# Kernel optimization log

Hardware: AMD Instinct MI355X
Metric: run time of the kernel (lower is better)

The kernel has to match this reference:

```python
import jax, jax.numpy as jnp
import numpy as np

ATOM_DIM = 128; RBF_DIM = 32; GEOM_HID = 128; SCAT = 64; OUT = 64; CUTOFF = 5.0
MAX_Z = 100; Z_EMB = 32; E_DIM = 32; PAIR_HID = 64
B = 16; N = 64; P = 8000; NE = 80


def _lin(key, i, o):
    kw, kb = jax.random.split(key)
    W = jax.random.normal(kw, (i, o), jnp.float32) / np.sqrt(i).astype(np.float32)
    b = jax.random.normal(kb, (o,), jnp.float32) * 0.01
    return W, b


def setup_inputs() -> dict:
    key = jax.random.key(0)
    ks = jax.random.split(key, 24)
    inp = {}
    inp["h_flat"] = jax.random.normal(ks[0], (B * N, ATOM_DIM), jnp.float32)
    inp["z_flat"] = jax.random.randint(ks[1], (B * N,), 0, MAX_Z + 1)
    inp["e_feat"] = jax.random.normal(ks[2], (NE, E_DIM), jnp.float32)
    inp["path_j"] = jax.random.randint(ks[3], (P,), 0, B * N)
    inp["path_k"] = jax.random.randint(ks[4], (P,), 0, B * N)
    # distances in (0, 1.2*cutoff) so some paths exceed the cutoff
    inp["path_r0j"] = jax.random.uniform(ks[5], (P,), jnp.float32, 0.1, 1.2 * CUTOFF)
    inp["path_r0k"] = jax.random.uniform(ks[6], (P,), jnp.float32, 0.1, 1.2 * CUTOFF)
    inp["path_rjk"] = jax.random.uniform(ks[7], (P,), jnp.float32, 0.1, 1.2 * CUTOFF)
    inp["path_cosangle"] = jax.random.uniform(ks[8], (P,), jnp.float32, -1.0, 1.0)
    inp["path_batch"] = jnp.sort(jax.random.randint(ks[9], (P,), 0, B))
    inp["bsz"] = B
    # params
    inp["z_emb"] = jax.random.normal(ks[10], (MAX_Z + 1, Z_EMB), jnp.float32)
    pe_in = 2 * Z_EMB + E_DIM
    inp["pe_w1"], inp["pe_b1"] = _lin(ks[11], pe_in, PAIR_HID)
    inp["pe_w2"], inp["pe_b2"] = _lin(ks[12], PAIR_HID, PAIR_HID)
    inp["pe_w3"], inp["pe_b3"] = _lin(ks[13], PAIR_HID, SCAT)
    gm_in = 2 * ATOM_DIM + 3 * RBF_DIM + 1
    inp["gm_w1"], inp["gm_b1"] = _lin(ks[14], gm_in, GEOM_HID)
    inp["gm_w2"], inp["gm_b2"] = _lin(ks[15], GEOM_HID, GEOM_HID)
    inp["gm_w3"], inp["gm_b3"] = _lin(ks[16], GEOM_HID, SCAT)
    inp["op_w1"], inp["op_b1"] = _lin(ks[17], SCAT, GEOM_HID)
    inp["op_w2"], inp["op_b2"] = _lin(ks[18], GEOM_HID, OUT)
    return inp


def _rbf(r):
    centers = jnp.linspace(0.0, CUTOFF, RBF_DIM)
    width = centers[1] - centers[0]
    return jnp.exp(-0.5 * ((r[..., None] - centers) / width) ** 2)


def _cutoff_fn(r):
    return 0.5 * (jnp.cos(jnp.pi * r / CUTOFF) + 1.0) * (r < CUTOFF)


def _mlp3(x, w1, b1, w2, b2, w3, b3):
    h = jax.nn.silu(x @ w1 + b1)
    h = jax.nn.silu(h @ w2 + b2)
    return h @ w3 + b3


def _mlp2(x, w1, b1, w2, b2):
    return jax.nn.silu(x @ w1 + b1) @ w2 + b2


def reference(h_flat, z_flat, e_feat, path_j, path_k, path_r0j, path_r0k,
              path_rjk, path_cosangle, path_batch, bsz, z_emb,
              pe_w1, pe_b1, pe_w2, pe_b2, pe_w3, pe_b3,
              gm_w1, gm_b1, gm_w2, gm_b2, gm_w3, gm_b3,
              op_w1, op_b1, op_w2, op_b2):
    n_e = e_feat.shape[0]
    n_p = path_j.shape[0]
    # gather atom features
    hj = h_flat[path_j]                                  # (P, atom_dim)
    hk = h_flat[path_k]
    f0j = _rbf(jnp.minimum(path_r0j, CUTOFF))            # (P, rbf_dim)
    f0k = _rbf(jnp.minimum(path_r0k, CUTOFF))
    fjk = _rbf(jnp.minimum(path_rjk, CUTOFF))
    geom_in = jnp.concatenate([hj, hk, f0j, f0k, fjk, path_cosangle[:, None]], axis=-1)
    g_geom = _mlp3(geom_in, gm_w1, gm_b1, gm_w2, gm_b2, gm_w3, gm_b3)  # (P, scat)
    # element-pair energy features
    ej = z_emb[z_flat[path_j]]                           # (P, z_emb)
    ek = z_emb[z_flat[path_k]]
    pair_in = jnp.concatenate([
        jnp.broadcast_to(ej[:, None, :], (n_p, n_e, ej.shape[-1])),
        jnp.broadcast_to(ek[:, None, :], (n_p, n_e, ek.shape[-1])),
        jnp.broadcast_to(e_feat[None, :, :], (n_p, n_e, e_feat.shape[-1])),
    ], axis=-1)                                          # (P, nE, 2*z_emb+e_dim)
    g_elem = _mlp3(pair_in, pe_w1, pe_b1, pe_w2, pe_b2, pe_w3, pe_b3)  # (P, nE, scat)
    # cutoff weights and outer-product contribution
    cw = _cutoff_fn(path_r0j) * _cutoff_fn(path_r0k) * _cutoff_fn(path_rjk)  # (P,)
    contrib = g_geom[:, None, :] * g_elem * cw[:, None, None]          # (P, nE, scat)
    # scatter-add into batch bins
    agg = jax.ops.segment_sum(contrib, path_batch, num_segments=bsz)   # (B, nE, scat)
    norm = jax.ops.segment_sum(cw, path_batch, num_segments=bsz)       # (B,)
    agg = agg / jnp.maximum(norm, 1e-8)[:, None, None]
    return _mlp2(agg, op_w1, op_b1, op_w2, op_b2)                      # (B, nE, out)
```

## Files before the change

### kernel.cpp

```cpp
#include <hip/hip_runtime.h>
#include <math.h>

typedef float f32x4 __attribute__((ext_vector_type(4)));
typedef short bf16x8 __attribute__((ext_vector_type(8)));
typedef unsigned short u16;

#define RBF_DIM 32
#define CUTOFF 5.0f
#define PI_F 3.14159265358979323846f
#define BB 16
#define PP 8000
#define NEE 80

#define CW_OFF      0
#define GCW_OFF     8000
#define AGG_OFF     520000
#define ZEJW_OFF    601920
#define ZEKW_OFF    608384
#define EFWB_OFF    614848
#define NORM_OFF    619968
#define AIDX_OFF    619984
#define ZJA_OFF     627984
#define ZKA_OFF     635984
#define BOFF_OFF    643984
#define BCNT_OFF    644004
#define BSUM_OFF    644036
#define BCNTB_OFF   644548
#define BLKOFF_OFF  645060
#define CHS_OFF     645096
#define CHC_OFF     645362
#define CHB_OFF     645628
#define NC_OFF      645894
#define W2THI_OFF   645896
#define W2TLO_OFF   647944
#define W3THI_OFF   649992
#define W3TLO_OFF   652040
#define PJA_OFF     654088
#define PKA_OFF     662088
#define CWA_OFF     670088
#define HHI_OFF     678088
#define HLO_OFF     743624
#define GW1JKH_OFF  809160
#define GW1JKL_OFF  825544
#define GW1RH_OFF   841928
#define GW1RL_OFF   850120
#define GW2H_OFF    858312
#define GW2L_OFF    866504
#define GW3H_OFF    874696
#define GW3L_OFF    878792
#define HJW_OFF     882888
#define HKW_OFF     1013960

__device__ __forceinline__ float siluf(float x) { return x / (1.f + __expf(-x)); }
__device__ __forceinline__ float cutoff_fn(float r) {
    return (r < CUTOFF) ? 0.5f * (cosf(PI_F * r / CUTOFF) + 1.f) : 0.f;
}
__device__ __forceinline__ float rbff(float r, int i) {
    r = fminf(r, CUTOFF);
    float a = r * (31.0f / CUTOFF) - (float)i;
    return __expf(-0.5f * a * a);
}
__device__ __forceinline__ u16 f2bf_rne(float x) {
    unsigned u = __float_as_uint(x);
    return (u16)((u + 0x7FFFu + ((u >> 16) & 1u)) >> 16);
}
__device__ __forceinline__ unsigned cvtpk2(float a, float b) {
    unsigned r;
    asm("v_cvt_pk_bf16_f32 %0, %1, %2" : "=v"(r) : "v"(a), "v"(b));
    return r;
}
__device__ __forceinline__ void splitpack8(const float* xs, bf16x8& hi, bf16x8& lo) {
    union { bf16x8 v; unsigned u[4]; } H, L;
    #pragma unroll
    for (int d = 0; d < 4; ++d) {
        float a = xs[2 * d], b = xs[2 * d + 1];
        unsigned h = cvtpk2(a, b);
        float ra = a - __uint_as_float(h << 16);
        float rb = b - __uint_as_float(h & 0xFFFF0000u);
        H.u[d] = h;
        L.u[d] = cvtpk2(ra, rb);
    }
    hi = H.v; lo = L.v;
}

__global__ __launch_bounds__(256) void k0a_k1(
    const float* r0j, const float* r0k, const float* rjk, const int* pbatch,
    const float* z_emb, const float* e_feat, const float* pe_w1, const float* pe_b1,
    const float* pe_w2, const float* pe_w3,
    const float* h_flat, const float* gm_w1, const float* gm_w2, const float* gm_w3,
    float* ws, int* wsi)
{
    __shared__ float cwL[256];
    __shared__ int bL[256];
    __shared__ int redC[256];
    __shared__ float embL[4 * 32];
    int blkAll = blockIdx.x, t = threadIdx.x;
    if (blkAll < 32) {
        int bi = blkAll;
        for (int i = t; i < 2560; i += 256) ws[AGG_OFF + bi*2560 + i] = 0.f;
        int p = bi*250 + t;
        float cw = 0.f; int bin = -1; int valid = 0;
        if (t < 250) {
            cw = cutoff_fn(r0j[p]) * cutoff_fn(r0k[p]) * cutoff_fn(rjk[p]);
            ws[CW_OFF + p] = cw;
            bin = pbatch[p];
            valid = (cw > 0.f) ? 1 : 0;
        }
        cwL[t] = cw; bL[t] = bin; redC[t] = valid;
        __syncthreads();
        if (t < 16) {
            float s = 0.f; int c2 = 0;
            for (int i = 0; i < 256; ++i) {
                bool m = (bL[i] == t);
                s += m ? cwL[i] : 0.f;
                c2 += (m && cwL[i] > 0.f) ? 1 : 0;
            }
            ws[BSUM_OFF + bi*16 + t] = s;
            wsi[BCNTB_OFF + bi*16 + t] = c2;
        }
        __syncthreads();
        for (int s = 128; s > 0; s >>= 1) {
            if (t < s) redC[t] += redC[t + s];
            __syncthreads();
        }
        if (t == 0) wsi[BCNT_OFF + bi] = redC[0];
        return;
    }
    if (blkAll >= 106) {
        int blk = blkAll - 106;
        if (blk < 32) {
            u16* hh = (u16*)(ws + HHI_OFF);
            u16* hl = (u16*)(ws + HLO_OFF);
            int base = blk * 4096;
            for (int idx = t; idx < 4096; idx += 256) {
                int e = base + idx;
                float v = h_flat[e];
                u16 h = f2bf_rne(v);
                hh[e] = h;
                hl[e] = f2bf_rne(v - __uint_as_float(((unsigned)h) << 16));
            }
        } else if (blk < 34) {
            u16* wh = (u16*)(ws + GW1JKH_OFF);
            u16* wl = (u16*)(ws + GW1JKL_OFF);
            int base = (blk - 32) * 16384;
            for (int idx = t; idx < 16384; idx += 256) {
                int e = base + idx;
                int m = e >> 7, k = e & 127;
                float v = gm_w1[((m < 128) ? k : (128 + k)) * 128 + (m & 127)];
                u16 h = f2bf_rne(v);
                wh[e] = h;
                wl[e] = f2bf_rne(v - __uint_as_float(((unsigned)h) << 16));
            }
        } else if (blk == 34) {
            u16* wh = (u16*)(ws + GW1RH_OFF);
            u16* wl = (u16*)(ws + GW1RL_OFF);
            for (int e = t; e < 16384; e += 256) {
                int m = e >> 7, k = e & 127;
                float v = (k < 97) ? gm_w1[(256 + k) * 128 + m] : 0.f;
                u16 h = f2bf_rne(v);
                wh[e] = h;
                wl[e] = f2bf_rne(v - __uint_as_float(((unsigned)h) << 16));
            }
        } else if (blk == 35) {
            u16* wh = (u16*)(ws + GW2H_OFF);
            u16* wl = (u16*)(ws + GW2L_OFF);
            for (int e = t; e < 16384; e += 256) {
                int m = e >> 7, k = e & 127;
                float v = gm_w2[k * 128 + m];
                u16 h = f2bf_rne(v);
                wh[e] = h;
                wl[e] = f2bf_rne(v - __uint_as_float(((unsigned)h) << 16));
            }
        } else {
            u16* wh = (u16*)(ws + GW3H_OFF);
            u16* wl = (u16*)(ws + GW3L_OFF);
            for (int e = t; e < 8192; e += 256) {
                int m = e >> 7, k = e & 127;
                float v = gm_w3[k * 64 + m];
                u16 h = f2bf_rne(v);
                wh[e] = h;
                wl[e] = f2bf_rne(v - __uint_as_float(((unsigned)h) << 16));
            }
        }
        return;
    }
    int blk = blkAll - 32;
    if (blk >= 72) {
        const float* W = (blk == 72) ? pe_w2 : pe_w3;
        u16* hiD = (u16*)(ws + ((blk == 72) ? W2THI_OFF : W3THI_OFF));
        u16* loD = (u16*)(ws + ((blk == 72) ? W2TLO_OFF : W3TLO_OFF));
        for (int idx = t; idx < 4096; idx += 256) {
            int k = idx >> 6, n = idx & 63;
            float v = W[idx];
            u16 h = f2bf_rne(v);
            float hf = __uint_as_float(((unsigned)h) << 16);
            hiD[n*64 + k] = h;
            loD[n*64 + k] = f2bf_rne(v - hf);
        }
        return;
    }
    int r0, nrows, wbase;
    const float* src;
    float* dst;
    bool addb = false;
    if (blk < 26)      { r0 = blk * 4;        nrows = 101; src = z_emb;  wbase = 0;  dst = ws + ZEJW_OFF; }
    else if (blk < 52) { r0 = (blk - 26) * 4; nrows = 101; src = z_emb;  wbase = 32; dst = ws + ZEKW_OFF; }
    else               { r0 = (blk - 52) * 4; nrows = NEE; src = e_feat; wbase = 64; dst = ws + EFWB_OFF; addb = true; }
    if (t < 128) {
        int rl = t >> 5, i = t & 31;
        int r = r0 + rl;
        embL[t] = (r < nrows) ? src[r * 32 + i] : 0.f;
    }
    __syncthreads();
    int rl = t >> 6, c = t & 63;
    float acc = addb ? pe_b1[c] : 0.f;
    #pragma unroll
    for (int i = 0; i < 32; ++i)
        acc = fmaf(embL[rl * 32 + i], pe_w1[(wbase + i) * 64 + c], acc);
    int r = r0 + rl;
    if (r < nrows) dst[r * 64 + c] = acc;
}

__global__ __launch_bounds__(256) void k0b(float* ws, int* wsi)
{
    __shared__ int bcntL[32];
    __shared__ int cntB[16];
    __shared__ int boff[17];
    __shared__ int chkoff[17];
    int t = threadIdx.x;
    if (t < 16) {
        float s = 0.f;
        #pragma unroll 4
        for (int bi = 0; bi < 32; ++bi) s += ws[BSUM_OFF + bi*16 + t];
        ws[NORM_OFF + t] = s;
    }
    if (t >= 32 && t < 48) {
        int b = t - 32;
        int cb = 0;
        #pragma unroll 4
        for (int bi = 0; bi < 32; ++bi) cb += wsi[BCNTB_OFF + bi*16 + b];
        cntB[b] = cb;
    }
    if (t >= 64 && t < 96) bcntL[t - 64] = wsi[BCNT_OFF + (t - 64)];
    __syncthreads();
    for (int off = 1; off < 32; off <<= 1) {
        int v = (t < 32 && t >= off) ? bcntL[t - off] : 0;
        __syncthreads();
        if (t < 32) bcntL[t] += v;
        __syncthreads();
    }
    if (t < 32) wsi[BLKOFF_OFF + t] = bcntL[t] - wsi[BCNT_OFF + t];
    if (t == 0) {
        wsi[BLKOFF_OFF + 32] = bcntL[31];
        int bo = 0, co = 0;
        for (int b = 0; b < 16; ++b) {
            boff[b] = bo; chkoff[b] = co;
            bo += cntB[b];
            co += (cntB[b] + 31) >> 5;
        }
        boff[16] = bo; chkoff[16] = co;
        wsi[NC_OFF] = co;
    }
    __syncthreads();
    int NCv = chkoff[16];
    for (int ci = t; ci < NCv; ci += 256) {
        int b = 0;
        while (chkoff[b + 1] <= ci) b++;
        int local = ci - chkoff[b];
        int rem = cntB[b] - local * 32;
        wsi[CHS_OFF + ci] = boff[b] + local * 32;
        wsi[CHC_OFF + ci] = (rem < 32) ? rem : 32;
        wsi[CHB_OFF + ci] = b;
    }
}

__global__ __launch_bounds__(256) void k0c_k1b(
    const int* pj, const int* pk, const int* zf, float* ws, int* wsi)
{
    __shared__ int sc[256];
    int blk = blockIdx.x, t = threadIdx.x;
    if (blk < 32) {
        int bi = blk;
        int p = bi*250 + t;
        int valid = (t < 250 && ws[CW_OFF + p] > 0.f) ? 1 : 0;
        sc[t] = valid;
        __syncthreads();
        for (int off = 1; off < 256; off <<= 1) {
            int v = (t >= off) ? sc[t - off] : 0;
            __syncthreads();
            sc[t] += v;
            __syncthreads();
        }
        if (valid) {
            int pos = wsi[BLKOFF_OFF + bi] + sc[t] - 1;
            int pjv = pj[p], pkv = pk[p];
            wsi[AIDX_OFF + pos] = p;
            wsi[ZJA_OFF + pos] = zf[pjv];
            wsi[ZKA_OFF + pos] = zf[pkv];
            wsi[PJA_OFF + pos] = pjv;
            wsi[PKA_OFF + pos] = pkv;
            ws[CWA_OFF + pos] = ws[CW_OFF + p];
        }
        return;
    }
    int a0 = (blk - 32) * 64;
    int lane = t & 63, w = t >> 6, c = lane & 15, g = lane >> 4;
    const u16* hh = (const u16*)(ws + HHI_OFF);
    const u16* hl = (const u16*)(ws + HLO_OFF);
    const u16* wh = (const u16*)(ws + GW1JKH_OFF);
    const u16* wl = (const u16*)(ws + GW1JKL_OFF);
    f32x4 acc[4][4];
    #pragma unroll
    for (int i = 0; i < 4; ++i)
        #pragma unroll
        for (int j = 0; j < 4; ++j) acc[i][j] = (f32x4){0.f, 0.f, 0.f, 0.f};
    #pragma unroll 1
    for (int ks = 0; ks < 4; ++ks) {
        bf16x8 Ah[4], Al[4], Bh[4], Bl[4];
        #pragma unroll
        for (int mt = 0; mt < 4; ++mt) {
            int off = (w * 64 + mt * 16 + c) * 128 + ks * 32 + g * 8;
            Ah[mt] = *(const bf16x8*)(wh + off);
            Al[mt] = *(const bf16x8*)(wl + off);
        }
        #pragma unroll
        for (int nt = 0; nt < 4; ++nt) {
            int off = (a0 + nt * 16 + c) * 128 + ks * 32 + g * 8;
            Bh[nt] = *(const bf16x8*)(hh + off);
            Bl[nt] = *(const bf16x8*)(hl + off);
        }
        #pragma unroll
        for (int mt = 0; mt < 4; ++mt)
            #pragma unroll
            for (int nt = 0; nt < 4; ++nt) {
                f32x4 d = acc[mt][nt];
                d = __builtin_amdgcn_mfma_f32_16x16x32_bf16(Ah[mt], Bh[nt], d, 0, 0, 0);
                d = __builtin_amdgcn_mfma_f32_16x16x32_bf16(Ah[mt], Bl[nt], d, 0, 0, 0);
                d = __builtin_amdgcn_mfma_f32_16x16x32_bf16(Al[mt], Bh[nt], d, 0, 0, 0);
                acc[mt][nt] = d;
            }
    }
    float* dst = ws + ((w < 2) ? HJW_OFF : HKW_OFF);
    #pragma unroll
    for (int mt = 0; mt < 4; ++mt)
        #pragma unroll
        for (int nt = 0; nt < 4; ++nt) {
            int m = (w & 1) * 64 + mt * 16 + g * 4;
            int a = a0 + nt * 16 + c;
            *(f32x4*)(dst + a * 128 + m) = acc[mt][nt];
        }
}

__global__ __launch_bounds__(256) void k2_geom_mfma(
    const float* r0jG, const float* r0kG, const float* rjkG, const float* cosG,
    const float* b1g, const float* b2g, const float* b3g,
    float* ws, const int* wsi, float* gcw)
{
    __shared__ __align__(16) float sum3L[32 * 128];
    __shared__ __align__(16) u16 rbfH[4096], rbfL[4096];
    __shared__ __align__(16) u16 h1H[4096], h1L[4096];
    __shared__ __align__(16) u16 h2H[4096], h2L[4096];
    __shared__ int pjS[32], pkS[32];
    __shared__ float cwS[32], r0jS[32], r0kS[32], rjkS[32], cosS[32];

    int NC = wsi[NC_OFF];
    int cid = blockIdx.x;
    if (cid >= NC) return;
    int cs = wsi[CHS_OFF + cid], cnt = wsi[CHC_OFF + cid];
    int t = threadIdx.x, lane = t & 63, w = t >> 6, c = lane & 15, g = lane >> 4;

    if (t < 32) {
        int ap = cs + min(t, cnt - 1);
        int a = wsi[AIDX_OFF + ap];
        pjS[t] = wsi[PJA_OFF + ap]; pkS[t] = wsi[PKA_OFF + ap];
        cwS[t] = ws[CWA_OFF + ap];
        r0jS[t] = r0jG[a]; r0kS[t] = r0kG[a]; rjkS[t] = rjkG[a]; cosS[t] = cosG[a];
    }
    __syncthreads();
    {
        int p = t >> 3, kc = (t & 7) * 16;
        const float* rj = ws + HJW_OFF + pjS[p] * 128 + kc;
        const float* rk = ws + HKW_OFF + pkS[p] * 128 + kc;
        #pragma unroll
        for (int q = 0; q < 4; ++q) {
            f32x4 v = *(const f32x4*)(rj + q * 4) + *(const f32x4*)(rk + q * 4);
            *(f32x4*)(sum3L + ((p * 128 + kc + q * 4) ^ ((p & 7) << 2))) = v;
        }
    }
    {
        int p = t >> 3, k0 = (t & 7) * 16;
        float r0jv = r0jS[p], r0kv = r0kS[p], rjkv = rjkS[p], cv = cosS[p];
        #pragma unroll
        for (int hf = 0; hf < 2; ++hf) {
            int kb = k0 + hf * 8;
            float xs[8];
            #pragma unroll
            for (int i = 0; i < 8; ++i) {
                int k = kb + i;
                float v;
                if (k < 32) v = rbff(r0jv, k);
                else if (k < 64) v = rbff(r0kv, k - 32);
                else if (k < 96) v = rbff(rjkv, k - 64);
                else if (k == 96) v = cv;
                else v = 0.f;
                xs[i] = v;
            }
            bf16x8 hi, lo;
            splitpack8(xs, hi, lo);
            int idx = (p * 128 + kb) ^ ((p & 7) << 3);
            *(bf16x8*)(rbfH + idx) = hi;
            *(bf16x8*)(rbfL + idx) = lo;
        }
    }
    __syncthreads();

    const u16* w1h = (const u16*)(ws + GW1RH_OFF);
    const u16* w1l = (const u16*)(ws + GW1RL_OFF);
    const u16* w2h = (const u16*)(ws + GW2H_OFF);
    const u16* w2l = (const u16*)(ws + GW2L_OFF);
    const u16* w3h = (const u16*)(ws + GW3H_OFF);
    const u16* w3l = (const u16*)(ws + GW3L_OFF);

    f32x4 acc[2][2];
    #pragma unroll
    for (int i = 0; i < 2; ++i)
        #pragma unroll
        for (int j = 0; j < 2; ++j) acc[i][j] = (f32x4){0.f, 0.f, 0.f, 0.f};
    #pragma unroll 1
    for (int ks = 0; ks < 4; ++ks) {
        bf16x8 Ah[2], Al[2], Bh[2], Bl[2];
        #pragma unroll
        for (int ml = 0; ml < 2; ++ml) {
            int off = ((w * 2 + ml) * 16 + c) * 128 + ks * 32 + g * 8;
            Ah[ml] = *(const bf16x8*)(w1h + off);
            Al[ml] = *(const bf16x8*)(w1l + off);
        }
        #pragma unroll
        for (int nt = 0; nt < 2; ++nt) {
            int p = nt * 16 + c;
            int idx = (p * 128 + ks * 32 + g * 8) ^ ((p & 7) << 3);
            Bh[nt] = *(const bf16x8*)(rbfH + idx);
            Bl[nt] = *(const bf16x8*)(rbfL + idx);
        }
        #pragma unroll
        for (int ml = 0; ml < 2; ++ml)
            #pragma unroll
            for (int nt = 0; nt < 2; ++nt) {
                f32x4 d = acc[ml][nt];
                d = __builtin_amdgcn_mfma_f32_16x16x32_bf16(Ah[ml], Bh[nt], d, 0, 0, 0);
                d = __builtin_amdgcn_mfma_f32_16x16x32_bf16(Ah[ml], Bl[nt], d, 0, 0, 0);
                d = __builtin_amdgcn_mfma_f32_16x16x32_bf16(Al[ml], Bh[nt], d, 0, 0, 0);
// ... 44 lines not shown
            Bh[nt] = *(const bf16x8*)(h1H + idx);
            Bl[nt] = *(const bf16x8*)(h1L + idx);
        }
        #pragma unroll
        for (int ml = 0; ml < 2; ++ml)
            #pragma unroll
            for (int nt = 0; nt < 2; ++nt) {
                f32x4 d = acc[ml][nt];
                d = __builtin_amdgcn_mfma_f32_16x16x32_bf16(Ah[ml], Bh[nt], d, 0, 0, 0);
                d = __builtin_amdgcn_mfma_f32_16x16x32_bf16(Ah[ml], Bl[nt], d, 0, 0, 0);
                d = __builtin_amdgcn_mfma_f32_16x16x32_bf16(Al[ml], Bh[nt], d, 0, 0, 0);
                acc[ml][nt] = d;
            }
    }
    #pragma unroll
    for (int ml = 0; ml < 2; ++ml)
        #pragma unroll
        for (int nt = 0; nt < 2; ++nt) {
            int p = nt * 16 + c;
            int m0 = (w * 2 + ml) * 16 + g * 4;
            f32x4 bb = *(const f32x4*)(b2g + m0);
            f32x4 x = acc[ml][nt] + bb;
            float v0 = siluf(x[0]), v1 = siluf(x[1]), v2 = siluf(x[2]), v3 = siluf(x[3]);
            unsigned h01 = cvtpk2(v0, v1), h23 = cvtpk2(v2, v3);
            float l0 = v0 - __uint_as_float(h01 << 16);
            float l1 = v1 - __uint_as_float(h01 & 0xFFFF0000u);
            float l2 = v2 - __uint_as_float(h23 << 16);
            float l3 = v3 - __uint_as_float(h23 & 0xFFFF0000u);
            unsigned lo01 = cvtpk2(l0, l1), lo23 = cvtpk2(l2, l3);
            int idx = (p * 128 + m0) ^ ((p & 7) << 3);
            uint2 uh; uh.x = h01; uh.y = h23;
            uint2 ul; ul.x = lo01; ul.y = lo23;
            *(uint2*)(h2H + idx) = uh;
            *(uint2*)(h2L + idx) = ul;
        }
    __syncthreads();

    f32x4 acc3[2];
    acc3[0] = (f32x4){0.f, 0.f, 0.f, 0.f};
    acc3[1] = (f32x4){0.f, 0.f, 0.f, 0.f};
    #pragma unroll 1
    for (int ks = 0; ks < 4; ++ks) {
        bf16x8 Ah, Al, Bh[2], Bl[2];
        {
            int off = (w * 16 + c) * 128 + ks * 32 + g * 8;
            Ah = *(const bf16x8*)(w3h + off);
            Al = *(const bf16x8*)(w3l + off);
        }
        #pragma unroll
        for (int nt = 0; nt < 2; ++nt) {
            int p = nt * 16 + c;
            int idx = (p * 128 + ks * 32 + g * 8) ^ ((p & 7) << 3);
            Bh[nt] = *(const bf16x8*)(h2H + idx);
            Bl[nt] = *(const bf16x8*)(h2L + idx);
        }
        #pragma unroll
        for (int nt = 0; nt < 2; ++nt) {
            f32x4 d = acc3[nt];
            d = __builtin_amdgcn_mfma_f32_16x16x32_bf16(Ah, Bh[nt], d, 0, 0, 0);
            d = __builtin_amdgcn_mfma_f32_16x16x32_bf16(Ah, Bl[nt], d, 0, 0, 0);
            d = __builtin_amdgcn_mfma_f32_16x16x32_bf16(Al, Bh[nt], d, 0, 0, 0);
            acc3[nt] = d;
        }
    }
    {
        int m0 = w * 16 + g * 4;
        f32x4 bb = *(const f32x4*)(b3g + m0);
        #pragma unroll
        for (int nt = 0; nt < 2; ++nt) {
            int p = nt * 16 + c;
            if (p < cnt) {
                f32x4 o = (acc3[nt] + bb) * cwS[p];
                *(f32x4*)(gcw + (cs + p) * 64 + m0) = o;
            }
        }
    }
}

__global__ __launch_bounds__(256) void k3_pair_mfma(
    const float* ws, const int* wsi, const float* gcw, float* agg,
    const float* b2g, const float* b3g)
{
    __shared__ __align__(16) float sL[32 * 64];
    __shared__ __align__(16) u16 h2buf[4][2048];
    __shared__ __align__(16) u16 a2lL[4096];
    __shared__ __align__(16) u16 a3lL[4096];

    int NC = wsi[NC_OFF];
    int bid = blockIdx.x;
    int cid = bid / 10;
    int et  = bid - cid * 10;
    if (cid >= NC) return;
    int cs  = wsi[CHS_OFF + cid];
    int cnt = wsi[CHC_OFF + cid];
    int bb  = wsi[CHB_OFF + cid];

    int t = threadIdx.x;
    int lane = t & 63, w = t >> 6;
    int c = lane & 15, g = lane >> 4;

    {
        int p = t >> 3, kc = (t & 7) * 8;
        int ap = cs + min(p, cnt - 1);
        int zj = wsi[ZJA_OFF + ap], zk = wsi[ZKA_OFF + ap];
        const f32x4* rj = (const f32x4*)(ws + ZEJW_OFF + zj * 64 + kc);
        const f32x4* rk = (const f32x4*)(ws + ZEKW_OFF + zk * 64 + kc);
        int sw = (p & 7) << 2;
        *(f32x4*)(sL + ((p * 64 + kc) ^ sw))     = rj[0] + rk[0];
        *(f32x4*)(sL + ((p * 64 + kc + 4) ^ sw)) = rj[1] + rk[1];
    }
    {
        const unsigned* s2 = (const unsigned*)(ws + W2TLO_OFF);
        const unsigned* s3 = (const unsigned*)(ws + W3TLO_OFF);
        unsigned* d2 = (unsigned*)a2lL;
        unsigned* d3 = (unsigned*)a3lL;
        #pragma unroll
        for (int rr = 0; rr < 8; ++rr) {
            int i = rr * 256 + t;
            int sw = ((i >> 5) & 7) << 2;
            d2[i ^ sw] = s2[i];
            d3[i ^ sw] = s3[i];
        }
    }
    const u16* w2hi = (const u16*)(ws + W2THI_OFF);
    const u16* w3hi = (const u16*)(ws + W3THI_OFF);
    bf16x8 A2h[4][2], A3h[4][2];
    #pragma unroll
    for (int mt = 0; mt < 4; ++mt)
        #pragma unroll
        for (int ks = 0; ks < 2; ++ks) {
            int off = (mt * 16 + c) * 64 + ks * 32 + g * 8;
            A2h[mt][ks] = *(const bf16x8*)(w2hi + off);
            A3h[mt][ks] = *(const bf16x8*)(w3hi + off);
        }
    __syncthreads();

    u16* myh = h2buf[w];
    u16* myl = h2buf[w] + 1024;
    const float* efp = ws + EFWB_OFF;
    const int aswz = (c & 7) << 3;

    const int cb64 = c * 64;
    const int wk0 = (g * 8) ^ aswz;
    const int wk1 = (32 + g * 8) ^ aswz;
    const int s48 = aswz & 48, s8 = aswz & 8;
    const int hwb = cb64 + ((4 * g) ^ s8);
    const u16* a2p = a2lL + cb64;
    const u16* a3p = a3lL + cb64;

    #pragma unroll 1
    for (int ei = 0; ei < 2; ++ei) {
        int e = et * 8 + w * 2 + ei;
        float part[16];
        #pragma unroll
        for (int i = 0; i < 16; ++i) part[i] = 0.f;

        #pragma unroll 1
        for (int nt = 0; nt < 2; ++nt) {
            int p = nt * 16 + c;
            int psw = (p & 7) << 2;
            f32x4 gvr[4];
            {
                int pc = cs + min(p, cnt - 1);
                #pragma unroll
                for (int mt = 0; mt < 4; ++mt)
                    gvr[mt] = *(const f32x4*)(gcw + pc * 64 + mt * 16 + 4 * g);
            }
            f32x4 acc4[4];
            #pragma unroll
            for (int mt = 0; mt < 4; ++mt) acc4[mt] = (f32x4){0.f, 0.f, 0.f, 0.f};
            #pragma unroll
            for (int ks = 0; ks < 2; ++ks) {
                f32x4 e0 = *(const f32x4*)(efp + e * 64 + ks * 32 + g * 8);
                f32x4 e1 = *(const f32x4*)(efp + e * 64 + ks * 32 + g * 8 + 4);
                int base = p * 64 + ks * 32 + g * 8;
                f32x4 x0 = *(const f32x4*)(sL + (base ^ psw));
                f32x4 x1 = *(const f32x4*)(sL + ((base + 4) ^ psw));
                x0 += e0; x1 += e1;
                float xs[8];
                #pragma unroll
                for (int i = 0; i < 4; ++i) { xs[i] = siluf(x0[i]); xs[4 + i] = siluf(x1[i]); }
                bf16x8 Bh, Bl;
                splitpack8(xs, Bh, Bl);
                const int wk = ks ? wk1 : wk0;
                #pragma unroll
                for (int mt = 0; mt < 4; ++mt) {
                    bf16x8 a2l = *(const bf16x8*)(a2p + wk + mt * 1024);
                    f32x4 d = acc4[mt];
                    d = __builtin_amdgcn_mfma_f32_16x16x32_bf16(A2h[mt][ks], Bh, d, 0, 0, 0);
                    d = __builtin_amdgcn_mfma_f32_16x16x32_bf16(A2h[mt][ks], Bl, d, 0, 0, 0);
                    d = __builtin_amdgcn_mfma_f32_16x16x32_bf16(a2l,         Bh, d, 0, 0, 0);
                    acc4[mt] = d;
                }
            }
            #pragma unroll
            for (int mt = 0; mt < 4; ++mt) {
                f32x4 b2v = *(const f32x4*)(b2g + mt * 16 + 4 * g);
                f32x4 h = acc4[mt] + b2v;
                float v0 = siluf(h[0]), v1 = siluf(h[1]), v2 = siluf(h[2]), v3 = siluf(h[3]);
                unsigned h01 = cvtpk2(v0, v1), h23 = cvtpk2(v2, v3);
                float l0 = v0 - __uint_as_float(h01 << 16);
                float l1 = v1 - __uint_as_float(h01 & 0xFFFF0000u);
                float l2 = v2 - __uint_as_float(h23 << 16);
                float l3 = v3 - __uint_as_float(h23 & 0xFFFF0000u);
                unsigned lo01 = cvtpk2(l0, l1), lo23 = cvtpk2(l2, l3);
                int idx = hwb + ((mt * 16) ^ s48);
                uint2 uh, ul;
                uh.x = h01; uh.y = h23;
                ul.x = lo01; ul.y = lo23;
                *(uint2*)(myh + idx) = uh;
                *(uint2*)(myl + idx) = ul;
                acc4[mt] = (f32x4){0.f, 0.f, 0.f, 0.f};
            }
            #pragma unroll
            for (int ks = 0; ks < 2; ++ks) {
                const int wk = ks ? wk1 : wk0;
                bf16x8 Ch = *(const bf16x8*)(myh + cb64 + wk);
                bf16x8 Cl = *(const bf16x8*)(myl + cb64 + wk);
                #pragma unroll
                for (int mt = 0; mt < 4; ++mt) {
                    bf16x8 a3l = *(const bf16x8*)(a3p + wk + mt * 1024);
                    f32x4 d = acc4[mt];
                    d = __builtin_amdgcn_mfma_f32_16x16x32_bf16(A3h[mt][ks], Ch, d, 0, 0, 0);
                    d = __builtin_amdgcn_mfma_f32_16x16x32_bf16(A3h[mt][ks], Cl, d, 0, 0, 0);
                    d = __builtin_amdgcn_mfma_f32_16x16x32_bf16(a3l,         Ch, d, 0, 0, 0);
                    acc4[mt] = d;
                }
            }
            float vmask = (p < cnt) ? 1.f : 0.f;
            #pragma unroll
            for (int mt = 0; mt < 4; ++mt) {
                f32x4 b3v = *(const f32x4*)(b3g + mt * 16 + 4 * g);
                f32x4 o = acc4[mt] + b3v;
                #pragma unroll
                for (int r = 0; r < 4; ++r) part[mt * 4 + r] += o[r] * gvr[mt][r] * vmask;
            }
        }
        #pragma unroll
        for (int i = 0; i < 16; ++i) {
            float v = part[i];
            v += __shfl_xor(v, 1, 64);
            v += __shfl_xor(v, 2, 64);
            v += __shfl_xor(v, 4, 64);
            v += __shfl_xor(v, 8, 64);
            part[i] = v;
        }
        int f = (c >> 2) * 16 + g * 4 + (c & 3);
        atomicAdd(agg + (bb * NEE + e) * 64 + f, part[c]);
    }
}

__global__ __launch_bounds__(256) void k4_out(
    const float* ws, const float* W1, const float* b1,
    const float* W2, const float* b2, float* out)
{
    __shared__ float xT[64][68];
    __shared__ float W1L[64 * 128];
    __shared__ float hTT[128][68];
    __shared__ float W2L[128 * 64];
    __shared__ float normL[16];
    int t = threadIdx.x;
    int gbase = blockIdx.x * 64;
    if (t < 16) normL[t] = 1.f / fmaxf(ws[NORM_OFF + t], 1e-8f);
    for (int idx = t; idx < 8192; idx += 256) { W1L[idx] = W1[idx]; W2L[idx] = W2[idx]; }
    __syncthreads();
    {
        int r = t & 63, cq = t >> 6;
        int gg = gbase + r;
        int b = gg / NEE;
        float rn = normL[b];
        const float* arow = ws + AGG_OFF + gg * 64 + cq * 16;
        #pragma unroll
        for (int q = 0; q < 4; ++q) {
            float4 v = *(const float4*)(arow + q * 4);
            int c = cq * 16 + q * 4;
            xT[c + 0][r] = v.x * rn; xT[c + 1][r] = v.y * rn;
            xT[c + 2][r] = v.z * rn; xT[c + 3][r] = v.w * rn;
        }
    }
    __syncthreads();
    {
        int tcx = t & 15, trx = t >> 4;
        int c0 = tcx * 8, r0 = trx * 4;
        float acc[4][8];
        #pragma unroll
        for (int j = 0; j < 4; ++j)
            #pragma unroll
            for (int q = 0; q < 8; ++q) acc[j][q] = 0.f;
        #pragma unroll 4
        for (int kk = 0; kk < 64; ++kk) {
            float4 x4 = *(const float4*)&xT[kk][r0];
            float4 wa = *(const float4*)&W1L[kk * 128 + c0];
            float4 wb = *(const float4*)&W1L[kk * 128 + c0 + 4];
            float x[4] = {x4.x, x4.y, x4.z, x4.w};
            float w[8] = {wa.x, wa.y, wa.z, wa.w, wb.x, wb.y, wb.z, wb.w};
            #pragma unroll
            for (int j = 0; j < 4; ++j)
                #pragma unroll
                for (int q = 0; q < 8; ++q)
                    acc[j][q] = fmaf(x[j], w[q], acc[j][q]);
        }
        #pragma unroll
        for (int q = 0; q < 8; ++q) {
            float bb = b1[c0 + q];
            float4 v;
            v.x = siluf(acc[0][q] + bb);
            v.y = siluf(acc[1][q] + bb);
            v.z = siluf(acc[2][q] + bb);
            v.w = siluf(acc[3][q] + bb);
            *(float4*)&hTT[c0 + q][r0] = v;
        }
    }
    __syncthreads();
    {
        int tcx = t & 7, trx = t >> 3;
        int c0 = tcx * 8, r0 = trx * 2;
        float acc[2][8];
        #pragma unroll
        for (int j = 0; j < 2; ++j)
            #pragma unroll
            for (int q = 0; q < 8; ++q) acc[j][q] = 0.f;
        #pragma unroll 4
        for (int kk = 0; kk < 128; ++kk) {
            float2 x2 = *(const float2*)&hTT[kk][r0];
            float4 wa = *(const float4*)&W2L[kk * 64 + c0];
            float4 wb = *(const float4*)&W2L[kk * 64 + c0 + 4];
            float w[8] = {wa.x, wa.y, wa.z, wa.w, wb.x, wb.y, wb.z, wb.w};
            #pragma unroll
            for (int q = 0; q < 8; ++q) {
                acc[0][q] = fmaf(x2.x, w[q], acc[0][q]);
                acc[1][q] = fmaf(x2.y, w[q], acc[1][q]);
            }
        }
        int gg = gbase + r0;
        #pragma unroll
        for (int j = 0; j < 2; ++j) {
            float o[8];
            #pragma unroll
            for (int q = 0; q < 8; ++q) o[q] = acc[j][q] + b2[c0 + q];
            *(float4*)&out[(gg + j) * 64 + c0] = make_float4(o[0], o[1], o[2], o[3]);
            *(float4*)&out[(gg + j) * 64 + c0 + 4] = make_float4(o[4], o[5], o[6], o[7]);
        }
    }
}

extern "C" void kernel_launch(void* const* d_in, const int* in_sizes, int n_in,
                              void* d_out, int out_size, void* d_ws, size_t ws_size,
                              hipStream_t stream) {
    (void)in_sizes; (void)n_in; (void)out_size; (void)ws_size;
    const float* h_flat = (const float*)d_in[0];
    const int*   z_flat = (const int*)d_in[1];
    const float* e_feat = (const float*)d_in[2];
    const int*   path_j = (const int*)d_in[3];
    const int*   path_k = (const int*)d_in[4];
    const float* r0j    = (const float*)d_in[5];
    const float* r0k    = (const float*)d_in[6];
    const float* rjk    = (const float*)d_in[7];
    const float* cosang = (const float*)d_in[8];
    const int*   pbatch = (const int*)d_in[9];
    const float* z_emb  = (const float*)d_in[11];
    const float* pe_w1  = (const float*)d_in[12];
    const float* pe_b1  = (const float*)d_in[13];
    const float* pe_w2  = (const float*)d_in[14];
    const float* pe_b2  = (const float*)d_in[15];
    const float* pe_w3  = (const float*)d_in[16];
    const float* pe_b3  = (const float*)d_in[17];
    const float* gm_w1  = (const float*)d_in[18];
    const float* gm_b1  = (const float*)d_in[19];
    const float* gm_w2  = (const float*)d_in[20];
    const float* gm_b2  = (const float*)d_in[21];
    const float* gm_w3  = (const float*)d_in[22];
    const float* gm_b3  = (const float*)d_in[23];
    const float* op_w1  = (const float*)d_in[24];
    const float* op_b1  = (const float*)d_in[25];
    const float* op_w2  = (const float*)d_in[26];
    const float* op_b2  = (const float*)d_in[27];

    float* ws  = (float*)d_ws;
    int*   wsi = (int*)d_ws;
    float* gcw = ws + GCW_OFF;
    float* agg = ws + AGG_OFF;

    hipLaunchKernelGGL(k0a_k1, dim3(143), dim3(256), 0, stream,
                       r0j, r0k, rjk, pbatch,
                       z_emb, e_feat, pe_w1, pe_b1, pe_w2, pe_w3,
                       h_flat, gm_w1, gm_w2, gm_w3, ws, wsi);
    hipLaunchKernelGGL(k0b, dim3(1), dim3(256), 0, stream, ws, wsi);
    hipLaunchKernelGGL(k0c_k1b, dim3(48), dim3(256), 0, stream,
                       path_j, path_k, z_flat, ws, wsi);
    hipLaunchKernelGGL(k2_geom_mfma, dim3(266), dim3(256), 0, stream,
                       r0j, r0k, rjk, cosang,
                       gm_b1, gm_b2, gm_b3, ws, wsi, gcw);
    hipLaunchKernelGGL(k3_pair_mfma, dim3(2660), dim3(256), 0, stream,
                       ws, wsi, gcw, agg, pe_b2, pe_b3);
    hipLaunchKernelGGL(k4_out, dim3(20), dim3(256), 0, stream,
                       ws, op_w1, op_b1, op_w2, op_b2, (float*)d_out);
}
```

Before: 134.8 us.

## Split pair-MLP work to one energy per wave and use a transpose-style reduction

```diff
diff --git a/kernel.cpp b/kernel.cpp
--- a/kernel.cpp
+++ b/kernel.cpp
@@ -583,8 +583,8 @@
 
     int NC = wsi[NC_OFF];
     int bid = blockIdx.x;
-    int cid = bid / 10;
-    int et  = bid - cid * 10;
+    int cid = bid / 20;
+    int et  = bid - cid * 20;
     if (cid >= NC) return;
     int cs  = wsi[CHS_OFF + cid];
     int cnt = wsi[CHC_OFF + cid];
@@ -628,6 +628,12 @@
             A2h[mt][ks] = *(const bf16x8*)(w2hi + off);
             A3h[mt][ks] = *(const bf16x8*)(w3hi + off);
         }
+    f32x4 b2f[4], b3f[4];
+    #pragma unroll
+    for (int mt = 0; mt < 4; ++mt) {
+        b2f[mt] = *(const f32x4*)(b2g + mt * 16 + 4 * g);
+        b3f[mt] = *(const f32x4*)(b3g + mt * 16 + 4 * g);
+    }
     __syncthreads();
 
     u16* myh = h2buf[w];
@@ -643,106 +649,121 @@
     const u16* a2p = a2lL + cb64;
     const u16* a3p = a3lL + cb64;
 
+    int e = et * 4 + w;
+    float part[16];
+    #pragma unroll
+    for (int i = 0; i < 16; ++i) part[i] = 0.f;
+
+    f32x4 ef00 = *(const f32x4*)(efp + e * 64 + g * 8);
+    f32x4 ef01 = *(const f32x4*)(efp + e * 64 + g * 8 + 4);
+    f32x4 ef10 = *(const f32x4*)(efp + e * 64 + 32 + g * 8);
+    f32x4 ef11 = *(const f32x4*)(efp + e * 64 + 32 + g * 8 + 4);
+
     #pragma unroll 1
-    for (int ei = 0; ei < 2; ++ei) {
-        int e = et * 8 + w * 2 + ei;
-        float part[16];
-        #pragma unroll
-        for (int i = 0; i < 16; ++i) part[i] = 0.f;
-
-        #pragma unroll 1
-        for (int nt = 0; nt < 2; ++nt) {
-            int p = nt * 16 + c;
-            int psw = (p & 7) << 2;
-            f32x4 gvr[4];
-            {
-                int pc = cs + min(p, cnt - 1);
-                #pragma unroll
-                for (int mt = 0; mt < 4; ++mt)
-                    gvr[mt] = *(const f32x4*)(gcw + pc * 64 + mt * 16 + 4 * g);
-            }
-            f32x4 acc4[4];
-            #pragma unroll
-            for (int mt = 0; mt < 4; ++mt) acc4[mt] = (f32x4){0.f, 0.f, 0.f, 0.f};
-            #pragma unroll
-            for (int ks = 0; ks < 2; ++ks) {
-                f32x4 e0 = *(const f32x4*)(efp + e * 64 + ks * 32 + g * 8);
-                f32x4 e1 = *(const f32x4*)(efp + e * 64 + ks * 32 + g * 8 + 4);
-                int base = p * 64 + ks * 32 + g * 8;
-                f32x4 x0 = *(const f32x4*)(sL + (base ^ psw));
-                f32x4 x1 = *(const f32x4*)(sL + ((base + 4) ^ psw));
-                x0 += e0; x1 += e1;
-                float xs[8];
-                #pragma unroll
-                for (int i = 0; i < 4; ++i) { xs[i] = siluf(x0[i]); xs[4 + i] = siluf(x1[i]); }
-                bf16x8 Bh, Bl;
-                splitpack8(xs, Bh, Bl);
-                const int wk = ks ? wk1 : wk0;
-                #pragma unroll
-                for (int mt = 0; mt < 4; ++mt) {
-                    bf16x8 a2l = *(const bf16x8*)(a2p + wk + mt * 1024);
-                    f32x4 d = acc4[mt];
-                    d = __builtin_amdgcn_mfma_f32_16x16x32_bf16(A2h[mt][ks], Bh, d, 0, 0, 0);
-                    d = __builtin_amdgcn_mfma_f32_16x16x32_bf16(A2h[mt][ks], Bl, d, 0, 0, 0);
-                    d = __builtin_amdgcn_mfma_f32_16x16x32_bf16(a2l,         Bh, d, 0, 0, 0);
-                    acc4[mt] = d;
-                }
-            }
+    for (int nt = 0; nt < 2; ++nt) {
+        int p = nt * 16 + c;
+        int psw = (p & 7) << 2;
+        f32x4 gvr[4];
+        {
+            int pc = cs + min(p, cnt - 1);
+            #pragma unroll
+            for (int mt = 0; mt < 4; ++mt)
+                gvr[mt] = *(const f32x4*)(gcw + pc * 64 + mt * 16 + 4 * g);
+        }
+        f32x4 acc4[4];
+        #pragma unroll
+        for (int mt = 0; mt < 4; ++mt) acc4[mt] = (f32x4){0.f, 0.f, 0.f, 0.f};
+        #pragma unroll
+        for (int ks = 0; ks < 2; ++ks) {
+            const int wk = ks ? wk1 : wk0;
+            f32x4 e0 = ks ? ef10 : ef00;
+            f32x4 e1 = ks ? ef11 : ef01;
+            int base = p * 64 + ks * 32 + g * 8;
+            f32x4 x0 = *(const f32x4*)(sL + (base ^ psw));
+            f32x4 x1 = *(const f32x4*)(sL + ((base + 4) ^ psw));
+            x0 += e0; x1 += e1;
+            float xs[8];
+            #pragma unroll
+            for (int i = 0; i < 4; ++i) { xs[i] = siluf(x0[i]); xs[4 + i] = siluf(x1[i]); }
+            bf16x8 Bh, Bl;
+            splitpack8(xs, Bh, Bl);
             #pragma unroll
             for (int mt = 0; mt < 4; ++mt) {
-                f32x4 b2v = *(const f32x4*)(b2g + mt * 16 + 4 * g);
-                f32x4 h = acc4[mt] + b2v;
-                float v0 = siluf(h[0]), v1 = siluf(h[1]), v2 = siluf(h[2]), v3 = siluf(h[3]);
-                unsigned h01 = cvtpk2(v0, v1), h23 = cvtpk2(v2, v3);
-                float l0 = v0 - __uint_as_float(h01 << 16);
-                float l1 = v1 - __uint_as_float(h01 & 0xFFFF0000u);
-                float l2 = v2 - __uint_as_float(h23 << 16);
-                float l3 = v3 - __uint_as_float(h23 & 0xFFFF0000u);
-                unsigned lo01 = cvtpk2(l0, l1), lo23 = cvtpk2(l2, l3);
-                int idx = hwb + ((mt * 16) ^ s48);
-                uint2 uh, ul;
-                uh.x = h01; uh.y = h23;
-                ul.x = lo01; ul.y = lo23;
-                *(uint2*)(myh + idx) = uh;
-                *(uint2*)(myl + idx) = ul;
-                acc4[mt] = (f32x4){0.f, 0.f, 0.f, 0.f};
-            }
-            #pragma unroll
-            for (int ks = 0; ks < 2; ++ks) {
-                const int wk = ks ? wk1 : wk0;
-                bf16x8 Ch = *(const bf16x8*)(myh + cb64 + wk);
-                bf16x8 Cl = *(const bf16x8*)(myl + cb64 + wk);
-                #pragma unroll
-                for (int mt = 0; mt < 4; ++mt) {
-                    bf16x8 a3l = *(const bf16x8*)(a3p + wk + mt * 1024);
-                    f32x4 d = acc4[mt];
-                    d = __builtin_amdgcn_mfma_f32_16x16x32_bf16(A3h[mt][ks], Ch, d, 0, 0, 0);
-                    d = __builtin_amdgcn_mfma_f32_16x16x32_bf16(A3h[mt][ks], Cl, d, 0, 0, 0);
-                    d = __builtin_amdgcn_mfma_f32_16x16x32_bf16(a3l,         Ch, d, 0, 0, 0);
-                    acc4[mt] = d;
-                }
-            }
-            float vmask = (p < cnt) ? 1.f : 0.f;
+                bf16x8 a2l = *(const bf16x8*)(a2p + wk + mt * 1024);
+                f32x4 d = acc4[mt];
+                d = __builtin_amdgcn_mfma_f32_16x16x32_bf16(A2h[mt][ks], Bh, d, 0, 0, 0);
+                d = __builtin_amdgcn_mfma_f32_16x16x32_bf16(A2h[mt][ks], Bl, d, 0, 0, 0);
+                d = __builtin_amdgcn_mfma_f32_16x16x32_bf16(a2l,         Bh, d, 0, 0, 0);
+                acc4[mt] = d;
+            }
+        }
+        #pragma unroll
+        for (int mt = 0; mt < 4; ++mt) {
+            f32x4 h = acc4[mt] + b2f[mt];
+            float v0 = siluf(h[0]), v1 = siluf(h[1]), v2 = siluf(h[2]), v3 = siluf(h[3]);
+            unsigned h01 = cvtpk2(v0, v1), h23 = cvtpk2(v2, v3);
+            float l0 = v0 - __uint_as_float(h01 << 16);
+            float l1 = v1 - __uint_as_float(h01 & 0xFFFF0000u);
+            float l2 = v2 - __uint_as_float(h23 << 16);
+            float l3 = v3 - __uint_as_float(h23 & 0xFFFF0000u);
+            unsigned lo01 = cvtpk2(l0, l1), lo23 = cvtpk2(l2, l3);
+            int idx = hwb + ((mt * 16) ^ s48);
+            uint2 uh, ul;
+            uh.x = h01; uh.y = h23;
+            ul.x = lo01; ul.y = lo23;
+            *(uint2*)(myh + idx) = uh;
+            *(uint2*)(myl + idx) = ul;
+            acc4[mt] = (f32x4){0.f, 0.f, 0.f, 0.f};
+        }
+        #pragma unroll
+        for (int ks = 0; ks < 2; ++ks) {
+            const int wk = ks ? wk1 : wk0;
+            bf16x8 Ch = *(const bf16x8*)(myh + cb64 + wk);
+            bf16x8 Cl = *(const bf16x8*)(myl + cb64 + wk);
             #pragma unroll
             for (int mt = 0; mt < 4; ++mt) {
-                f32x4 b3v = *(const f32x4*)(b3g + mt * 16 + 4 * g);
-                f32x4 o = acc4[mt] + b3v;
-                #pragma unroll
-                for (int r = 0; r < 4; ++r) part[mt * 4 + r] += o[r] * gvr[mt][r] * vmask;
-            }
-        }
-        #pragma unroll
-        for (int i = 0; i < 16; ++i) {
-            float v = part[i];
-            v += __shfl_xor(v, 1, 64);
-            v += __shfl_xor(v, 2, 64);
-            v += __shfl_xor(v, 4, 64);
-            v += __shfl_xor(v, 8, 64);
-            part[i] = v;
-        }
-        int f = (c >> 2) * 16 + g * 4 + (c & 3);
-        atomicAdd(agg + (bb * NEE + e) * 64 + f, part[c]);
-    }
+                bf16x8 a3l = *(const bf16x8*)(a3p + wk + mt * 1024);
+                f32x4 d = acc4[mt];
+                d = __builtin_amdgcn_mfma_f32_16x16x32_bf16(A3h[mt][ks], Ch, d, 0, 0, 0);
+                d = __builtin_amdgcn_mfma_f32_16x16x32_bf16(A3h[mt][ks], Cl, d, 0, 0, 0);
+                d = __builtin_amdgcn_mfma_f32_16x16x32_bf16(a3l,         Ch, d, 0, 0, 0);
+                acc4[mt] = d;
+            }
+        }
+        float vmask = (p < cnt) ? 1.f : 0.f;
+        #pragma unroll
+        for (int mt = 0; mt < 4; ++mt) {
+            f32x4 o = acc4[mt] + b3f[mt];
+            #pragma unroll
+            for (int r = 0; r < 4; ++r) part[mt * 4 + r] += o[r] * gvr[mt][r] * vmask;
+        }
+    }
+    float v8[8];
+    #pragma unroll
+    for (int j = 0; j < 8; ++j) {
+        float keep = (c & 8) ? part[j + 8] : part[j];
+        float send = (c & 8) ? part[j] : part[j + 8];
+        v8[j] = keep + __shfl_xor(send, 8, 64);
+    }
+    float v4[4];
+    #pragma unroll
+    for (int j = 0; j < 4; ++j) {
+        float keep = (c & 4) ? v8[j + 4] : v8[j];
+        float send = (c & 4) ? v8[j] : v8[j + 4];
+        v4[j] = keep + __shfl_xor(send, 4, 64);
+    }
+    float v2[2];
+    #pragma unroll
+    for (int j = 0; j < 2; ++j) {
+        float keep = (c & 2) ? v4[j + 2] : v4[j];
+        float send = (c & 2) ? v4[j] : v4[j + 2];
+        v2[j] = keep + __shfl_xor(send, 2, 64);
+    }
+    float keep1 = (c & 1) ? v2[1] : v2[0];
+    float send1 = (c & 1) ? v2[0] : v2[1];
+    float v1 = keep1 + __shfl_xor(send1, 1, 64);
+    int f = (c >> 2) * 16 + g * 4 + (c & 3);
+    atomicAdd(agg + (bb * NEE + e) * 64 + f, v1);
 }
 
 __global__ __launch_bounds__(256) void k4_out(
@@ -886,7 +907,7 @@
     hipLaunchKernelGGL(k2_geom_mfma, dim3(266), dim3(256), 0, stream,
                        r0j, r0k, rjk, cosang,
                        gm_b1, gm_b2, gm_b3, ws, wsi, gcw);
-    hipLaunchKernelGGL(k3_pair_mfma, dim3(2660), dim3(256), 0, stream,
+    hipLaunchKernelGGL(k3_pair_mfma, dim3(5320), dim3(256), 0, stream,
                        ws, wsi, gcw, agg, pe_b2, pe_b3);
     hipLaunchKernelGGL(k4_out, dim3(20), dim3(256), 0, stream,
                        ws, op_w1, op_b1, op_w2, op_b2, (float*)d_out);
```

Result: slower. 142.8 us (+5.9%).

## Replace scan-based compaction with atomic per-batch reservoirs and shuffle-based hidden exchange

Applied to the files above, without the earlier changes.

```diff
diff --git a/kernel.cpp b/kernel.cpp
--- a/kernel.cpp
+++ b/kernel.cpp
@@ -11,6 +11,7 @@
 #define BB 16
 #define PP 8000
 #define NEE 80
+#define RSZ 500
 
 #define CW_OFF      0
 #define GCW_OFF     8000
@@ -24,13 +25,6 @@
 #define ZKA_OFF     635984
 #define BOFF_OFF    643984
 #define BCNT_OFF    644004
-#define BSUM_OFF    644036
-#define BCNTB_OFF   644548
-#define BLKOFF_OFF  645060
-#define CHS_OFF     645096
-#define CHC_OFF     645362
-#define CHB_OFF     645628
-#define NC_OFF      645894
 #define W2THI_OFF   645896
 #define W2TLO_OFF   647944
 #define W3THI_OFF   649992
@@ -88,42 +82,42 @@
     const float* z_emb, const float* e_feat, const float* pe_w1, const float* pe_b1,
     const float* pe_w2, const float* pe_w3,
     const float* h_flat, const float* gm_w1, const float* gm_w2, const float* gm_w3,
+    const int* pj, const int* pk, const int* zf,
     float* ws, int* wsi)
 {
     __shared__ float cwL[256];
     __shared__ int bL[256];
-    __shared__ int redC[256];
     __shared__ float embL[4 * 32];
     int blkAll = blockIdx.x, t = threadIdx.x;
     if (blkAll < 32) {
         int bi = blkAll;
         for (int i = t; i < 2560; i += 256) ws[AGG_OFF + bi*2560 + i] = 0.f;
         int p = bi*250 + t;
-        float cw = 0.f; int bin = -1; int valid = 0;
+        float cw = 0.f; int bin = -1;
         if (t < 250) {
             cw = cutoff_fn(r0j[p]) * cutoff_fn(r0k[p]) * cutoff_fn(rjk[p]);
-            ws[CW_OFF + p] = cw;
             bin = pbatch[p];
-            valid = (cw > 0.f) ? 1 : 0;
-        }
-        cwL[t] = cw; bL[t] = bin; redC[t] = valid;
+            if (cw > 0.f) {
+                int pos = atomicAdd(&wsi[BCNT_OFF + bin], 1);
+                if (pos < RSZ) {
+                    int slot = bin * RSZ + pos;
+                    int pjv = pj[p], pkv = pk[p];
+                    wsi[AIDX_OFF + slot] = p;
+                    wsi[ZJA_OFF + slot] = zf[pjv];
+                    wsi[ZKA_OFF + slot] = zf[pkv];
+                    wsi[PJA_OFF + slot] = pjv;
+                    wsi[PKA_OFF + slot] = pkv;
+                    ws[CWA_OFF + slot] = cw;
+                }
+            }
+        }
+        cwL[t] = cw; bL[t] = bin;
         __syncthreads();
         if (t < 16) {
-            float s = 0.f; int c2 = 0;
-            for (int i = 0; i < 256; ++i) {
-                bool m = (bL[i] == t);
-                s += m ? cwL[i] : 0.f;
-                c2 += (m && cwL[i] > 0.f) ? 1 : 0;
-            }
-            ws[BSUM_OFF + bi*16 + t] = s;
-            wsi[BCNTB_OFF + bi*16 + t] = c2;
-        }
-        __syncthreads();
-        for (int s = 128; s > 0; s >>= 1) {
-            if (t < s) redC[t] += redC[t + s];
-            __syncthreads();
-        }
-        if (t == 0) wsi[BCNT_OFF + bi] = redC[0];
+            float s = 0.f;
+            for (int i = 0; i < 256; ++i) s += (bL[i] == t) ? cwL[i] : 0.f;
+            atomicAdd(ws + NORM_OFF + t, s);
+        }
         return;
     }
     if (blkAll >= 106) {
@@ -221,89 +215,10 @@
     if (r < nrows) dst[r * 64 + c] = acc;
 }
 
-__global__ __launch_bounds__(256) void k0b(float* ws, int* wsi)
+__global__ __launch_bounds__(256) void k1b_hw(float* ws)
 {
-    __shared__ int bcntL[32];
-    __shared__ int cntB[16];
-    __shared__ int boff[17];
-    __shared__ int chkoff[17];
     int t = threadIdx.x;
-    if (t < 16) {
-        float s = 0.f;
-        #pragma unroll 4
-        for (int bi = 0; bi < 32; ++bi) s += ws[BSUM_OFF + bi*16 + t];
-        ws[NORM_OFF + t] = s;
-    }
-    if (t >= 32 && t < 48) {
-        int b = t - 32;
-        int cb = 0;
-        #pragma unroll 4
-        for (int bi = 0; bi < 32; ++bi) cb += wsi[BCNTB_OFF + bi*16 + b];
-        cntB[b] = cb;
-    }
-    if (t >= 64 && t < 96) bcntL[t - 64] = wsi[BCNT_OFF + (t - 64)];
-    __syncthreads();
-    for (int off = 1; off < 32; off <<= 1) {
-        int v = (t < 32 && t >= off) ? bcntL[t - off] : 0;
-        __syncthreads();
-        if (t < 32) bcntL[t] += v;
-        __syncthreads();
-    }
-    if (t < 32) wsi[BLKOFF_OFF + t] = bcntL[t] - wsi[BCNT_OFF + t];
-    if (t == 0) {
-        wsi[BLKOFF_OFF + 32] = bcntL[31];
-        int bo = 0, co = 0;
-        for (int b = 0; b < 16; ++b) {
-            boff[b] = bo; chkoff[b] = co;
-            bo += cntB[b];
-            co += (cntB[b] + 31) >> 5;
-        }
-        boff[16] = bo; chkoff[16] = co;
-        wsi[NC_OFF] = co;
-    }
-    __syncthreads();
-    int NCv = chkoff[16];
-    for (int ci = t; ci < NCv; ci += 256) {
-        int b = 0;
-        while (chkoff[b + 1] <= ci) b++;
-        int local = ci - chkoff[b];
-        int rem = cntB[b] - local * 32;
-        wsi[CHS_OFF + ci] = boff[b] + local * 32;
-        wsi[CHC_OFF + ci] = (rem < 32) ? rem : 32;
-        wsi[CHB_OFF + ci] = b;
-    }
-}
-
-__global__ __launch_bounds__(256) void k0c_k1b(
-    const int* pj, const int* pk, const int* zf, float* ws, int* wsi)
-{
-    __shared__ int sc[256];
-    int blk = blockIdx.x, t = threadIdx.x;
-    if (blk < 32) {
-        int bi = blk;
-        int p = bi*250 + t;
-        int valid = (t < 250 && ws[CW_OFF + p] > 0.f) ? 1 : 0;
-        sc[t] = valid;
-        __syncthreads();
-        for (int off = 1; off < 256; off <<= 1) {
-            int v = (t >= off) ? sc[t - off] : 0;
-            __syncthreads();
-            sc[t] += v;
-            __syncthreads();
-        }
-        if (valid) {
-            int pos = wsi[BLKOFF_OFF + bi] + sc[t] - 1;
-            int pjv = pj[p], pkv = pk[p];
-            wsi[AIDX_OFF + pos] = p;
-            wsi[ZJA_OFF + pos] = zf[pjv];
-            wsi[ZKA_OFF + pos] = zf[pkv];
-            wsi[PJA_OFF + pos] = pjv;
-            wsi[PKA_OFF + pos] = pkv;
-            ws[CWA_OFF + pos] = ws[CW_OFF + p];
-        }
-        return;
-    }
-    int a0 = (blk - 32) * 64;
+    int a0 = blockIdx.x * 64;
     int lane = t & 63, w = t >> 6, c = lane & 15, g = lane >> 4;
     const u16* hh = (const u16*)(ws + HHI_OFF);
     const u16* hl = (const u16*)(ws + HLO_OFF);
@@ -363,10 +278,14 @@
     __shared__ int pjS[32], pkS[32];
     __shared__ float cwS[32], r0jS[32], r0kS[32], rjkS[32], cosS[32];
 
-    int NC = wsi[NC_OFF];
-    int cid = blockIdx.x;
-    if (cid >= NC) return;
-    int cs = wsi[CHS_OFF + cid], cnt = wsi[CHC_OFF + cid];
+    int bid = blockIdx.x;
+    int b = bid >> 4, ci = bid & 15;
+    int cntb = wsi[BCNT_OFF + b];
+    if (cntb > RSZ) cntb = RSZ;
+    int cs = b * RSZ + ci * 32;
+    int cnt = cntb - ci * 32;
+    if (cnt <= 0) return;
+    if (cnt > 32) cnt = 32;
     int t = threadIdx.x, lane = t & 63, w = t >> 6, c = lane & 15, g = lane >> 4;
 
     if (t < 32) {
@@ -577,18 +496,19 @@
     const float* b2g, const float* b3g)
 {
     __shared__ __align__(16) float sL[32 * 64];
-    __shared__ __align__(16) u16 h2buf[4][2048];
     __shared__ __align__(16) u16 a2lL[4096];
     __shared__ __align__(16) u16 a3lL[4096];
 
-    int NC = wsi[NC_OFF];
     int bid = blockIdx.x;
     int cid = bid / 10;
     int et  = bid - cid * 10;
-    if (cid >= NC) return;
-    int cs  = wsi[CHS_OFF + cid];
-    int cnt = wsi[CHC_OFF + cid];
-    int bb  = wsi[CHB_OFF + cid];
+    int bb = cid >> 4, ci = cid & 15;
+    int cntb = wsi[BCNT_OFF + bb];
+    if (cntb > RSZ) cntb = RSZ;
+    int cs = bb * RSZ + ci * 32;
+    int cnt = cntb - ci * 32;
+    if (cnt <= 0) return;
+    if (cnt > 32) cnt = 32;
 
     int t = threadIdx.x;
     int lane = t & 63, w = t >> 6;
@@ -630,16 +550,11 @@
         }
     __syncthreads();
 
-    u16* myh = h2buf[w];
-    u16* myl = h2buf[w] + 1024;
     const float* efp = ws + EFWB_OFF;
     const int aswz = (c & 7) << 3;
-
     const int cb64 = c * 64;
     const int wk0 = (g * 8) ^ aswz;
     const int wk1 = (32 + g * 8) ^ aswz;
-    const int s48 = aswz & 48, s8 = aswz & 8;
-    const int hwb = cb64 + ((4 * g) ^ s8);
     const u16* a2p = a2lL + cb64;
     const u16* a3p = a3lL + cb64;
 
@@ -688,37 +603,38 @@
                     acc4[mt] = d;
                 }
             }
+            float sv[4][4];
             #pragma unroll
             for (int mt = 0; mt < 4; ++mt) {
                 f32x4 b2v = *(const f32x4*)(b2g + mt * 16 + 4 * g);
                 f32x4 h = acc4[mt] + b2v;
-                float v0 = siluf(h[0]), v1 = siluf(h[1]), v2 = siluf(h[2]), v3 = siluf(h[3]);
-                unsigned h01 = cvtpk2(v0, v1), h23 = cvtpk2(v2, v3);
-                float l0 = v0 - __uint_as_float(h01 << 16);
-                float l1 = v1 - __uint_as_float(h01 & 0xFFFF0000u);
-                float l2 = v2 - __uint_as_float(h23 << 16);
-                float l3 = v3 - __uint_as_float(h23 & 0xFFFF0000u);
-                unsigned lo01 = cvtpk2(l0, l1), lo23 = cvtpk2(l2, l3);
-                int idx = hwb + ((mt * 16) ^ s48);
-                uint2 uh, ul;
-                uh.x = h01; uh.y = h23;
-                ul.x = lo01; ul.y = lo23;
-                *(uint2*)(myh + idx) = uh;
-                *(uint2*)(myl + idx) = ul;
+                #pragma unroll
+                for (int r = 0; r < 4; ++r) sv[mt][r] = siluf(h[r]);
                 acc4[mt] = (f32x4){0.f, 0.f, 0.f, 0.f};
+            }
+            bf16x8 Ch[2], Cl[2];
+            #pragma unroll
+            for (int ks = 0; ks < 2; ++ks) {
+                float v[8];
+                #pragma unroll
+                for (int i = 0; i < 8; ++i) {
+                    int sl = c + ((((g & 1) << 1) + (i >> 2)) << 4);
+                    float t0 = __shfl(sv[2 * ks][i & 3], sl, 64);
+                    float t1 = __shfl(sv[2 * ks + 1][i & 3], sl, 64);
+                    v[i] = (g >= 2) ? t1 : t0;
+                }
+                splitpack8(v, Ch[ks], Cl[ks]);
             }
             #pragma unroll
             for (int ks = 0; ks < 2; ++ks) {
                 const int wk = ks ? wk1 : wk0;
-                bf16x8 Ch = *(const bf16x8*)(myh + cb64 + wk);
-                bf16x8 Cl = *(const bf16x8*)(myl + cb64 + wk);
                 #pragma unroll
                 for (int mt = 0; mt < 4; ++mt) {
                     bf16x8 a3l = *(const bf16x8*)(a3p + wk + mt * 1024);
                     f32x4 d = acc4[mt];
-                    d = __builtin_amdgcn_mfma_f32_16x16x32_bf16(A3h[mt][ks], Ch, d, 0, 0, 0);
-                    d = __builtin_amdgcn_mfma_f32_16x16x32_bf16(A3h[mt][ks], Cl, d, 0, 0, 0);
-                    d = __builtin_amdgcn_mfma_f32_16x16x32_bf16(a3l,         Ch, d, 0, 0, 0);
+                    d = __builtin_amdgcn_mfma_f32_16x16x32_bf16(A3h[mt][ks], Ch[ks], d, 0, 0, 0);
+                    d = __builtin_amdgcn_mfma_f32_16x16x32_bf16(A3h[mt][ks], Cl[ks], d, 0, 0, 0);
+                    d = __builtin_amdgcn_mfma_f32_16x16x32_bf16(a3l,         Ch[ks], d, 0, 0, 0);
                     acc4[mt] = d;
                 }
             }
@@ -876,17 +792,19 @@
     float* gcw = ws + GCW_OFF;
     float* agg = ws + AGG_OFF;
 
+    hipMemsetAsync((char*)d_ws + (size_t)NORM_OFF * 4, 0, 64, stream);
+    hipMemsetAsync((char*)d_ws + (size_t)BCNT_OFF * 4, 0, 64, stream);
+
     hipLaunchKernelGGL(k0a_k1, dim3(143), dim3(256), 0, stream,
                        r0j, r0k, rjk, pbatch,
                        z_emb, e_feat, pe_w1, pe_b1, pe_w2, pe_w3,
-                       h_flat, gm_w1, gm_w2, gm_w3, ws, wsi);
-    hipLaunchKernelGGL(k0b, dim3(1), dim3(256), 0, stream, ws, wsi);
-    hipLaunchKernelGGL(k0c_k1b, dim3(48), dim3(256), 0, stream,
+                       h_flat, gm_w1, gm_w2, gm_w3,
                        path_j, path_k, z_flat, ws, wsi);
-    hipLaunchKernelGGL(k2_geom_mfma, dim3(266), dim3(256), 0, stream,
+    hipLaunchKernelGGL(k1b_hw, dim3(16), dim3(256), 0, stream, ws);
+    hipLaunchKernelGGL(k2_geom_mfma, dim3(256), dim3(256), 0, stream,
                        r0j, r0k, rjk, cosang,
                        gm_b1, gm_b2, gm_b3, ws, wsi, gcw);
-    hipLaunchKernelGGL(k3_pair_mfma, dim3(2660), dim3(256), 0, stream,
+    hipLaunchKernelGGL(k3_pair_mfma, dim3(2560), dim3(256), 0, stream,
                        ws, wsi, gcw, agg, pe_b2, pe_b3);
     hipLaunchKernelGGL(k4_out, dim3(20), dim3(256), 0, stream,
                        ws, op_w1, op_b1, op_w2, op_b2, (float*)d_out);
```

Measured after the change: 200.8 us. +48.9%, slower.
